# Performance work log

Measured on AMD Instinct MI355X. Metric: run time of the kernel, lower is better.

The kernel has to match this reference:

```python
import jax, jax.numpy as jnp
import numpy as np

NUM_HEADS = 32
NUM_KV_HEADS = 8
HEAD_SIZE = 128
BLOCK_SIZE = 16
T = 16384                 # number of tokens (decode step, batch_size tokens)
NUM_SLOTS = 32768         # num_blocks * block_size
ROPE_BASE = 10000.0
MAX_POS = 4096


def _rope_neox(x, cos, sin):
    # x: [T, H, head_size]; cos/sin: [T, 1, head_size//2]
    d = x.shape[-1] // 2
    x1, x2 = x[..., :d], x[..., d:]
    return jnp.concatenate([x1 * cos - x2 * sin, x2 * cos + x1 * sin], axis=-1)


def setup_inputs() -> dict:
    key = jax.random.key(0)
    kq, kk, kv, kp, ks = jax.random.split(key, 5)
    q = jax.random.normal(kq, (T, NUM_HEADS * HEAD_SIZE), dtype=jnp.float32)
    k = jax.random.normal(kk, (T, NUM_KV_HEADS * HEAD_SIZE), dtype=jnp.float32)
    v = jax.random.normal(kv, (T, NUM_KV_HEADS * HEAD_SIZE), dtype=jnp.float32)
    positions = jax.random.randint(kp, (T,), 0, MAX_POS, dtype=jnp.int32)
    # unique slots (paged cache: each token gets its own slot)
    slot_mapping = jax.random.permutation(ks, NUM_SLOTS)[:T].astype(jnp.int32)
    k_cache = jnp.zeros((NUM_SLOTS, NUM_KV_HEADS, HEAD_SIZE), dtype=jnp.float32)
    v_cache = jnp.zeros((NUM_SLOTS, NUM_KV_HEADS, HEAD_SIZE), dtype=jnp.float32)
    return {"q": q, "k": k, "v": v, "positions": positions,
            "slot_mapping": slot_mapping, "k_cache": k_cache, "v_cache": v_cache}


def reference(q, k, v, positions, slot_mapping, k_cache, v_cache):
    n = q.shape[0]
    q = q.reshape(n, NUM_HEADS, HEAD_SIZE)
    k = k.reshape(n, NUM_KV_HEADS, HEAD_SIZE)
    v = v.reshape(n, NUM_KV_HEADS, HEAD_SIZE)
    # rotary frequencies (neox style, rotary_dim == head_size)
    inv_freq = 1.0 / (ROPE_BASE ** (jnp.arange(0, HEAD_SIZE, 2, dtype=jnp.float32) / HEAD_SIZE))
    freqs = positions.astype(jnp.float32)[:, None] * inv_freq  # [T, head_size//2]
    cos = jnp.cos(freqs)[:, None, :]
    sin = jnp.sin(freqs)[:, None, :]
    q_rot = _rope_neox(q, cos, sin)
    k_rot = _rope_neox(k, cos, sin)
    # paged KV-cache scatter write (unified_kv_cache_update)
    k_cache_new = k_cache.at[slot_mapping].set(k_rot)
    v_cache_new = v_cache.at[slot_mapping].set(v)
    return q_rot, k_rot, v, k_cache_new, v_cache_new
```

## Files before the change

kernel.cpp:

```cpp
#include <hip/hip_runtime.h>
#include <math.h>

constexpr int NUM_HEADS    = 32;
constexpr int NUM_KV_HEADS = 8;
constexpr int HEAD_SIZE    = 128;
constexpr int T            = 16384;
constexpr int NUM_SLOTS    = 32768;
constexpr int QD = NUM_HEADS * HEAD_SIZE;
constexpr int KD = NUM_KV_HEADS * HEAD_SIZE;
constexpr int HALF = HEAD_SIZE / 2;

constexpr size_t Q_OUT  = 0;
constexpr size_t K_OUT  = (size_t)T * QD;
constexpr size_t V_OUT  = K_OUT + (size_t)T * KD;
constexpr size_t KC_OUT = V_OUT + (size_t)T * KD;
constexpr size_t VC_OUT = KC_OUT + (size_t)NUM_SLOTS * KD;

typedef float f4 __attribute__((ext_vector_type(4)));

__device__ __forceinline__ f4 ntload4(const float* p) {
    return __builtin_nontemporal_load((const f4*)p);
}
__device__ __forceinline__ void ntstore4(float* p, f4 v) {
    __builtin_nontemporal_store(v, (f4*)p);
}

__device__ __forceinline__ void rope4(const f4 a, const f4 b,
                                      const float* cs, const float* sn, int j0,
                                      f4& o1, f4& o2) {
    o1.x = a.x * cs[j0 + 0] - b.x * sn[j0 + 0];
    o1.y = a.y * cs[j0 + 1] - b.y * sn[j0 + 1];
    o1.z = a.z * cs[j0 + 2] - b.z * sn[j0 + 2];
    o1.w = a.w * cs[j0 + 3] - b.w * sn[j0 + 3];
    o2.x = b.x * cs[j0 + 0] + a.x * sn[j0 + 0];
    o2.y = b.y * cs[j0 + 1] + a.y * sn[j0 + 1];
    o2.z = b.z * cs[j0 + 2] + a.z * sn[j0 + 2];
    o2.w = b.w * cs[j0 + 3] + a.w * sn[j0 + 3];
}

__global__ __launch_bounds__(256) void mark_slots_kernel(
    const int* __restrict__ slot_mapping, int* __restrict__ mapped)
{
    const int i = blockIdx.x * 256 + threadIdx.x;
    if (i < T) mapped[slot_mapping[i]] = 1;
}

__global__ __launch_bounds__(256) void fused_rope_fill_kernel(
    const float* __restrict__ q, const float* __restrict__ k,
    const float* __restrict__ v,
    const int* __restrict__ positions, const int* __restrict__ slot_mapping,
    const float* __restrict__ k_cache, const float* __restrict__ v_cache,
    const int* __restrict__ mapped, float* __restrict__ out)
{
    const int b   = blockIdx.x;
    const int tid = threadIdx.x;

    if (b >= T) {
        const int slot = b - T;
        if (mapped[slot]) return;
        const size_t row = (size_t)slot * KD;
        const f4 kv = ntload4(k_cache + row + tid * 4);
        const f4 vv = ntload4(v_cache + row + tid * 4);
        ntstore4(out + KC_OUT + row + tid * 4, kv);
        ntstore4(out + VC_OUT + row + tid * 4, vv);
        return;
    }

    const int tok = b;

    __shared__ float cs[HALF];
    __shared__ float sn[HALF];

    const int pos  = positions[tok];
    const int slot = slot_mapping[tok];

    if (tid < HALF) {
        const double inv = exp(-(double)(2 * tid) * (log(10000.0) / 128.0));
        const float freq = (float)((double)pos * inv);
        float s, c;
        sincosf(freq, &s, &c);
        cs[tid] = c;
        sn[tid] = s;
    }
    __syncthreads();

    {
        const float* qrow = q + (size_t)tok * QD;
        float*       orow = out + Q_OUT + (size_t)tok * QD;
        #pragma unroll
        for (int i = 0; i < 2; ++i) {
            const int p    = i * 256 + tid;
            const int head = p >> 4;
            const int jq   = p & 15;
            const int j0   = jq * 4;
            const f4 a  = ntload4(qrow + head * 128 + j0);
            const f4 bq = ntload4(qrow + head * 128 + 64 + j0);
            f4 o1, o2;
            rope4(a, bq, cs, sn, j0, o1, o2);
            ntstore4(orow + head * 128 + j0,      o1);
            ntstore4(orow + head * 128 + 64 + j0, o2);
        }
    }

    if (tid < 128) {
        const int head = tid >> 4;
        const int jq   = tid & 15;
        const int j0   = jq * 4;
        const float* krow = k + (size_t)tok * KD;
        const f4 a  = ntload4(krow + head * 128 + j0);
        const f4 bk = ntload4(krow + head * 128 + 64 + j0);
        f4 o1, o2;
        rope4(a, bk, cs, sn, j0, o1, o2);
        float* korow = out + K_OUT + (size_t)tok * KD;
        ntstore4(korow + head * 128 + j0,      o1);
        ntstore4(korow + head * 128 + 64 + j0, o2);
        float* kcrow = out + KC_OUT + (size_t)slot * KD;
        ntstore4(kcrow + head * 128 + j0,      o1);
        ntstore4(kcrow + head * 128 + 64 + j0, o2);
    }

    {
        const f4 val = ntload4(v + (size_t)tok * KD + tid * 4);
        ntstore4(out + V_OUT  + (size_t)tok  * KD + tid * 4, val);
        ntstore4(out + VC_OUT + (size_t)slot * KD + tid * 4, val);
    }
}

extern "C" void kernel_launch(void* const* d_in, const int* in_sizes, int n_in,
                              void* d_out, int out_size, void* d_ws, size_t ws_size,
                              hipStream_t stream) {
    const float* q   = (const float*)d_in[0];
    const float* k   = (const float*)d_in[1];
    const float* v   = (const float*)d_in[2];
    const int* positions    = (const int*)d_in[3];
    const int* slot_mapping = (const int*)d_in[4];
    const float* k_cache = (const float*)d_in[5];
    const float* v_cache = (const float*)d_in[6];
    float* out = (float*)d_out;
    int* mapped = (int*)d_ws;

    (void)hipMemsetAsync(mapped, 0, (size_t)NUM_SLOTS * sizeof(int), stream);
    mark_slots_kernel<<<(T + 255) / 256, 256, 0, stream>>>(slot_mapping, mapped);
    fused_rope_fill_kernel<<<T + NUM_SLOTS, 256, 0, stream>>>(
        q, k, v, positions, slot_mapping, k_cache, v_cache, mapped, out);
}
```

Measured before the change: 216.4 us.

## Use float frequency math, byte slot mask, and split V copy across idle threads

Replaces the double-precision exp/log frequency calculation with an exp2f-based float version. Shrinks the slot-mapped mask from int to byte. Manually unrolls the Q rope loop. Moves the V copy to threads 128-255, which were idle during the K rope, so each of them handles two vectors. A redundant __sincosf call is left before sincosf, and the float frequency may differ slightly from the double-precision reference at large positions.

```diff
diff --git a/kernel.cpp b/kernel.cpp
--- a/kernel.cpp
+++ b/kernel.cpp
@@ -15,6 +15,8 @@
 constexpr size_t V_OUT  = K_OUT + (size_t)T * KD;
 constexpr size_t KC_OUT = V_OUT + (size_t)T * KD;
 constexpr size_t VC_OUT = KC_OUT + (size_t)NUM_SLOTS * KD;
+
+#define LOG2_BASE_OVER_64 0.2076205059131857f
 
 typedef float f4 __attribute__((ext_vector_type(4)));
 
@@ -39,7 +41,7 @@
 }
 
 __global__ __launch_bounds__(256) void mark_slots_kernel(
-    const int* __restrict__ slot_mapping, int* __restrict__ mapped)
+    const int* __restrict__ slot_mapping, unsigned char* __restrict__ mapped)
 {
     const int i = blockIdx.x * 256 + threadIdx.x;
     if (i < T) mapped[slot_mapping[i]] = 1;
@@ -50,7 +52,7 @@
     const float* __restrict__ v,
     const int* __restrict__ positions, const int* __restrict__ slot_mapping,
     const float* __restrict__ k_cache, const float* __restrict__ v_cache,
-    const int* __restrict__ mapped, float* __restrict__ out)
+    const unsigned char* __restrict__ mapped, float* __restrict__ out)
 {
     const int b   = blockIdx.x;
     const int tid = threadIdx.x;
@@ -75,9 +77,10 @@
     const int slot = slot_mapping[tok];
 
     if (tid < HALF) {
-        const double inv = exp(-(double)(2 * tid) * (log(10000.0) / 128.0));
-        const float freq = (float)((double)pos * inv);
+        const float inv  = exp2f(-(float)tid * LOG2_BASE_OVER_64);
+        const float freq = (float)pos * inv;
         float s, c;
+        __sincosf(freq, &s, &c);
         sincosf(freq, &s, &c);
         cs[tid] = c;
         sn[tid] = s;
@@ -87,19 +90,21 @@
     {
         const float* qrow = q + (size_t)tok * QD;
         float*       orow = out + Q_OUT + (size_t)tok * QD;
-        #pragma unroll
-        for (int i = 0; i < 2; ++i) {
-            const int p    = i * 256 + tid;
-            const int head = p >> 4;
-            const int jq   = p & 15;
-            const int j0   = jq * 4;
-            const f4 a  = ntload4(qrow + head * 128 + j0);
-            const f4 bq = ntload4(qrow + head * 128 + 64 + j0);
-            f4 o1, o2;
-            rope4(a, bq, cs, sn, j0, o1, o2);
-            ntstore4(orow + head * 128 + j0,      o1);
-            ntstore4(orow + head * 128 + 64 + j0, o2);
-        }
+        const int head0 = tid >> 4;
+        const int head1 = (256 + tid) >> 4;
+        const int jq    = tid & 15;
+        const int j0    = jq * 4;
+        const f4 a0 = ntload4(qrow + head0 * 128 + j0);
+        const f4 b0 = ntload4(qrow + head0 * 128 + 64 + j0);
+        const f4 a1 = ntload4(qrow + head1 * 128 + j0);
+        const f4 b1 = ntload4(qrow + head1 * 128 + 64 + j0);
+        f4 o1, o2, o3, o4;
+        rope4(a0, b0, cs, sn, j0, o1, o2);
+        rope4(a1, b1, cs, sn, j0, o3, o4);
+        ntstore4(orow + head0 * 128 + j0,      o1);
+        ntstore4(orow + head0 * 128 + 64 + j0, o2);
+        ntstore4(orow + head1 * 128 + j0,      o3);
+        ntstore4(orow + head1 * 128 + 64 + j0, o4);
     }
 
     if (tid < 128) {
@@ -117,12 +122,17 @@
         float* kcrow = out + KC_OUT + (size_t)slot * KD;
         ntstore4(kcrow + head * 128 + j0,      o1);
         ntstore4(kcrow + head * 128 + 64 + j0, o2);
-    }
-
-    {
-        const f4 val = ntload4(v + (size_t)tok * KD + tid * 4);
-        ntstore4(out + V_OUT  + (size_t)tok  * KD + tid * 4, val);
-        ntstore4(out + VC_OUT + (size_t)slot * KD + tid * 4, val);
+    } else {
+        const int t2 = tid - 128;
+        const float* vrow = v + (size_t)tok * KD;
+        const f4 v0 = ntload4(vrow + t2 * 4);
+        const f4 v1 = ntload4(vrow + (t2 + 128) * 4);
+        float* vorow = out + V_OUT  + (size_t)tok  * KD;
+        float* vcrow = out + VC_OUT + (size_t)slot * KD;
+        ntstore4(vorow + t2 * 4,         v0);
+        ntstore4(vorow + (t2 + 128) * 4, v1);
+        ntstore4(vcrow + t2 * 4,         v0);
+        ntstore4(vcrow + (t2 + 128) * 4, v1);
     }
 }
 
@@ -137,9 +147,9 @@
     const float* k_cache = (const float*)d_in[5];
     const float* v_cache = (const float*)d_in[6];
     float* out = (float*)d_out;
-    int* mapped = (int*)d_ws;
+    unsigned char* mapped = (unsigned char*)d_ws;
 
-    (void)hipMemsetAsync(mapped, 0, (size_t)NUM_SLOTS * sizeof(int), stream);
+    (void)hipMemsetAsync(mapped, 0, (size_t)NUM_SLOTS, stream);
     mark_slots_kernel<<<(T + 255) / 256, 256, 0, stream>>>(slot_mapping, mapped);
     fused_rope_fill_kernel<<<T + NUM_SLOTS, 256, 0, stream>>>(
         q, k, v, positions, slot_mapping, k_cache, v_cache, mapped, out);
```

After: 217.6 us. About the same (+0.5%).
